# Kernel optimization log

Hardware: AMD Instinct MI355X
Metric: run time of the kernel (lower is better)

Reference implementation:

```python
import jax, jax.numpy as jnp
import numpy as np

ALPHA = 0.2          # leaky_relu negative slope
NEG_INF = -9e15      # mask fill value (matches torch source)


def setup_inputs() -> dict:
    key = jax.random.key(0)
    k_h, k_mask, k_W, k_a = jax.random.split(key, 4)
    B, N, F_in, F_out = 4, 65536, 128, 128
    h = jax.random.normal(k_h, (B, N, F_in), dtype=jnp.float32)
    # op_mask > 0 means "mask out this neighbor" (prev/self/next)
    op_mask = jax.random.randint(k_mask, (B, N, 3), 0, 2, dtype=jnp.int32)
    # xavier_uniform-style init for params
    lim_W = 1.414 * np.sqrt(6.0 / (F_in + F_out))
    W = jax.random.uniform(k_W, (F_in, F_out), dtype=jnp.float32, minval=-lim_W, maxval=lim_W)
    lim_a = 1.414 * np.sqrt(6.0 / (2 * F_out + 1))
    a = jax.random.uniform(k_a, (2 * F_out, 1), dtype=jnp.float32, minval=-lim_a, maxval=lim_a)
    return {"h": h, "op_mask": op_mask, "W": W, "a": a}


def reference(h, op_mask, W, a):
    F_out = W.shape[1]
    Wh = jnp.matmul(h, W)                                   # [B, N, F]
    # windowed neighbors: prev (roll +1), self, next (roll -1)
    Wh_concat = jnp.stack(
        [jnp.roll(Wh, 1, axis=1), Wh, jnp.roll(Wh, -1, axis=1)], axis=-2
    )                                                       # [B, N, 3, F]
    Wh1 = jnp.matmul(Wh, a[:F_out])                         # [B, N, 1]
    Wh2 = jnp.matmul(Wh, a[F_out:])                         # [B, N, 1]
    Wh2_concat = jnp.stack(
        [jnp.roll(Wh2, 1, axis=1), Wh2, jnp.roll(Wh2, -1, axis=1)], axis=-1
    )                                                       # [B, N, 1, 3]
    e = jax.nn.leaky_relu(Wh1[..., None] + Wh2_concat, ALPHA)  # [B, N, 1, 3]
    e = jnp.where(op_mask[:, :, None, :] > 0, jnp.float32(NEG_INF), e)
    attention = jax.nn.softmax(e, axis=-1)                  # [B, N, 1, 3]
    # dropout_prob = 0.0 (eval-equivalent), so dropout is identity
    h_new = jnp.matmul(attention, Wh_concat).squeeze(-2)    # [B, N, F]
    return h_new
```

## Files before the change

kernel.cpp:

```cpp
#include <hip/hip_runtime.h>
#include <hip/hip_bf16.h>

typedef __attribute__((ext_vector_type(8))) short short8;
typedef __attribute__((ext_vector_type(4))) float f32x4;

#define ALPHA 0.2f
#define NEG_INF -9e15f
#define OUT_ROWS 126

__device__ __forceinline__ unsigned short f2bf(float x) {
    union { float f; unsigned int u; } v; v.f = x;
    unsigned int r = v.u + 0x7FFFu + ((v.u >> 16) & 1u);
    return (unsigned short)(r >> 16);
}

__global__ __launch_bounds__(256, 2)
void gat_fused(const float* __restrict__ h, const int* __restrict__ opm,
               const float* __restrict__ W, const float* __restrict__ a,
               float* __restrict__ out, int N) {
    __shared__ __align__(16) char smem[65536];
    __shared__ float a_s[256];
    __shared__ float wh1_s[128];
    __shared__ float wh2_s[128];
    __shared__ float att_s[128][4];

    const int t = threadIdx.x;
    const int b = blockIdx.y;
    const int row_start = blockIdx.x * OUT_ROWS;
    const int out_rows = min(OUT_ROWS, N - row_start);
    const float* hB = h + (size_t)b * N * 128;
    float* outB = out + (size_t)b * N * 128;

    a_s[t] = a[t];

    #pragma unroll
    for (int i = 0; i < 16; ++i) {
        int idx4 = t + i * 256;
        int k = idx4 >> 5;
        int n4 = (idx4 & 31) << 2;
        float4 w4 = *(const float4*)(W + (k << 7) + n4);
        unsigned short bf[4] = { f2bf(w4.x), f2bf(w4.y), f2bf(w4.z), f2bf(w4.w) };
        #pragma unroll
        for (int j = 0; j < 4; ++j) {
            int jj = j ^ (t & 3);
            int n = n4 + jj;
            *(unsigned short*)(smem + 32768 + n * 256 + ((k * 2) ^ ((n & 7) << 4))) = bf[jj];
        }
    }
    #pragma unroll
    for (int i = 0; i < 16; ++i) {
        int idx4 = t + i * 256;
        int r = idx4 >> 5;
        int c = (idx4 & 31) << 2;
        int g = row_start - 1 + r;
        if (g < 0) g += N;
        if (g >= N) g -= N;
        float4 h4 = *(const float4*)(hB + (size_t)g * 128 + c);
        ushort4 p = make_ushort4(f2bf(h4.x), f2bf(h4.y), f2bf(h4.z), f2bf(h4.w));
        *(ushort4*)(smem + r * 256 + ((c * 2) ^ ((r & 7) << 4))) = p;
    }
    __syncthreads();

    const int lane = t & 63;
    const int wave = t >> 6;
    const int wr = (wave >> 1) << 6;
    const int wc = (wave & 1) << 6;
    const int l15 = lane & 15;
    const int lg = (lane >> 4) & 3;

    f32x4 acc[4][4];
    #pragma unroll
    for (int mi = 0; mi < 4; ++mi)
        #pragma unroll
        for (int ni = 0; ni < 4; ++ni)
            acc[mi][ni] = (f32x4){0.f, 0.f, 0.f, 0.f};

    #pragma unroll
    for (int kk = 0; kk < 4; ++kk) {
        int kbyte = (kk << 6) + (lg << 4);
        short8 af[4], bfr[4];
        #pragma unroll
        for (int mi = 0; mi < 4; ++mi) {
            int m = wr + (mi << 4) + l15;
            af[mi] = *(const short8*)(smem + m * 256 + (kbyte ^ ((m & 7) << 4)));
        }
        #pragma unroll
        for (int ni = 0; ni < 4; ++ni) {
            int n = wc + (ni << 4) + l15;
            bfr[ni] = *(const short8*)(smem + 32768 + n * 256 + (kbyte ^ ((n & 7) << 4)));
        }
        #pragma unroll
        for (int mi = 0; mi < 4; ++mi)
            #pragma unroll
            for (int ni = 0; ni < 4; ++ni)
                acc[mi][ni] = __builtin_amdgcn_mfma_f32_16x16x32_bf16(
                    af[mi], bfr[ni], acc[mi][ni], 0, 0, 0);
    }
    __syncthreads();

    #pragma unroll
    for (int mi = 0; mi < 4; ++mi) {
        #pragma unroll
        for (int ni = 0; ni < 4; ++ni) {
            int col = wc + (ni << 4) + l15;
            #pragma unroll
            for (int j = 0; j < 4; ++j) {
                int row = wr + (mi << 4) + (lg << 2) + j;
                *(float*)(smem + row * 512 + ((col * 4) ^ ((row & 7) << 4))) = acc[mi][ni][j];
            }
        }
    }
    __syncthreads();

    {
        int r = t >> 1;
        int cb = (t & 1) << 6;
        float s1 = 0.f, s2 = 0.f;
        #pragma unroll
        for (int i = 0; i < 16; ++i) {
            int c = cb + (i << 2);
            f32x4 w4 = *(const f32x4*)(smem + r * 512 + ((c * 4) ^ ((r & 7) << 4)));
            s1 += w4[0] * a_s[c] + w4[1] * a_s[c + 1] + w4[2] * a_s[c + 2] + w4[3] * a_s[c + 3];
            s2 += w4[0] * a_s[128 + c] + w4[1] * a_s[129 + c] + w4[2] * a_s[130 + c] + w4[3] * a_s[131 + c];
        }
        s1 += __shfl_xor(s1, 1);
        s2 += __shfl_xor(s2, 1);
        if ((t & 1) == 0) { wh1_s[r] = s1; wh2_s[r] = s2; }
    }
    __syncthreads();

    if (t < 128) {
        int r = t;
        if (r >= 1 && r <= out_rows) {
            int g = row_start + r - 1;
            const int* mr = opm + ((size_t)b * N + g) * 3;
            float w1 = wh1_s[r];
            float e0 = w1 + wh2_s[r - 1];
            float e1 = w1 + wh2_s[r];
            float e2 = w1 + wh2_s[r + 1];
            e0 = e0 > 0.f ? e0 : ALPHA * e0;
            e1 = e1 > 0.f ? e1 : ALPHA * e1;
            e2 = e2 > 0.f ? e2 : ALPHA * e2;
            if (mr[0] > 0) e0 = NEG_INF;
            if (mr[1] > 0) e1 = NEG_INF;
            if (mr[2] > 0) e2 = NEG_INF;
            float m = fmaxf(e0, fmaxf(e1, e2));
            float x0 = expf(e0 - m), x1 = expf(e1 - m), x2 = expf(e2 - m);
            float inv = 1.f / (x0 + x1 + x2);
            att_s[r][0] = x0 * inv;
            att_s[r][1] = x1 * inv;
            att_s[r][2] = x2 * inv;
        }
    }
    __syncthreads();

    for (int it = 0; it < 16; ++it) {
        int r = 1 + (wave << 1) + ((lane >> 5) & 1) + (it << 3);
        if (r > out_rows) continue;
        int c = (lane & 31) << 2;
        float a0 = att_s[r][0], a1 = att_s[r][1], a2 = att_s[r][2];
        f32x4 wm = *(const f32x4*)(smem + (r - 1) * 512 + ((c * 4) ^ (((r - 1) & 7) << 4)));
        f32x4 w0 = *(const f32x4*)(smem + r * 512 + ((c * 4) ^ ((r & 7) << 4)));
        f32x4 wp = *(const f32x4*)(smem + (r + 1) * 512 + ((c * 4) ^ (((r + 1) & 7) << 4)));
        f32x4 res;
        #pragma unroll
        for (int j = 0; j < 4; ++j)
            res[j] = a0 * wm[j] + a1 * w0[j] + a2 * wp[j];
        int g = row_start + r - 1;
        *(f32x4*)(outB + (size_t)g * 128 + c) = res;
    }
}

extern "C" void kernel_launch(void* const* d_in, const int* in_sizes, int n_in,
                              void* d_out, int out_size, void* d_ws, size_t ws_size,
                              hipStream_t stream) {
    const float* h   = (const float*)d_in[0];
    const int*   opm = (const int*)d_in[1];
    const float* W   = (const float*)d_in[2];
    const float* a   = (const float*)d_in[3];
    float* out = (float*)d_out;
    const int N = 65536;
    const int B = 4;
    dim3 grid((N + OUT_ROWS - 1) / OUT_ROWS, B);
    gat_fused<<<grid, 256, 0, stream>>>(h, opm, W, a, out, N);
}
```

Before: 65.04 us.

## Prepack W into MFMA fragment layout and store Wh as bf16 in LDS

A small pre-kernel converts W to bf16 once and writes it to the workspace in the exact per-lane MFMA B-fragment order. The main kernel then loads B fragments straight from global memory instead of having every block transpose W into shared memory. The Wh tile is stored back to LDS as bf16 rather than fp32, which halves LDS to 32KB and allows launch bounds of 4 blocks per CU instead of 2. In exchange it adds a second launch and per-block global reads of W fragments, and rounding Wh to bf16 before the attention reductions and output loses precision.

```diff
diff --git a/kernel.cpp b/kernel.cpp
--- a/kernel.cpp
+++ b/kernel.cpp
@@ -13,12 +13,31 @@
     unsigned int r = v.u + 0x7FFFu + ((v.u >> 16) & 1u);
     return (unsigned short)(r >> 16);
 }
+__device__ __forceinline__ float bf2f(unsigned short x) {
+    union { unsigned int u; float f; } v; v.u = ((unsigned int)x) << 16;
+    return v.f;
+}
 
-__global__ __launch_bounds__(256, 2)
+__global__ void prep_wt(const float* __restrict__ W, unsigned short* __restrict__ ws) {
+    int q = blockIdx.x * 256 + threadIdx.x;
+    int lane = q & 63;
+    int fi = q >> 6;
+    int ni = fi & 3;
+    int kk = (fi >> 2) & 3;
+    int wcg = fi >> 4;
+    int n = wcg * 64 + ni * 16 + (lane & 15);
+    int k0 = kk * 32 + ((lane >> 4) & 3) * 8;
+    short8 o;
+    #pragma unroll
+    for (int j = 0; j < 8; ++j) o[j] = (short)f2bf(W[(k0 + j) * 128 + n]);
+    *(short8*)(ws + (size_t)q * 8) = o;
+}
+
+__global__ __launch_bounds__(256, 4)
 void gat_fused(const float* __restrict__ h, const int* __restrict__ opm,
-               const float* __restrict__ W, const float* __restrict__ a,
+               const unsigned short* __restrict__ ws, const float* __restrict__ a,
                float* __restrict__ out, int N) {
-    __shared__ __align__(16) char smem[65536];
+    __shared__ __align__(16) char smem[32768];
     __shared__ float a_s[256];
     __shared__ float wh1_s[128];
     __shared__ float wh2_s[128];
@@ -36,20 +55,6 @@
     #pragma unroll
     for (int i = 0; i < 16; ++i) {
         int idx4 = t + i * 256;
-        int k = idx4 >> 5;
-        int n4 = (idx4 & 31) << 2;
-        float4 w4 = *(const float4*)(W + (k << 7) + n4);
-        unsigned short bf[4] = { f2bf(w4.x), f2bf(w4.y), f2bf(w4.z), f2bf(w4.w) };
-        #pragma unroll
-        for (int j = 0; j < 4; ++j) {
-            int jj = j ^ (t & 3);
-            int n = n4 + jj;
-            *(unsigned short*)(smem + 32768 + n * 256 + ((k * 2) ^ ((n & 7) << 4))) = bf[jj];
-        }
-    }
-    #pragma unroll
-    for (int i = 0; i < 16; ++i) {
-        int idx4 = t + i * 256;
         int r = idx4 >> 5;
         int c = (idx4 & 31) << 2;
         int g = row_start - 1 + r;
@@ -64,7 +69,8 @@
     const int lane = t & 63;
     const int wave = t >> 6;
     const int wr = (wave >> 1) << 6;
-    const int wc = (wave & 1) << 6;
+    const int wcg = wave & 1;
+    const int wc = wcg << 6;
     const int l15 = lane & 15;
     const int lg = (lane >> 4) & 3;
 
@@ -75,19 +81,18 @@
         for (int ni = 0; ni < 4; ++ni)
             acc[mi][ni] = (f32x4){0.f, 0.f, 0.f, 0.f};
 
+    const short8* wsv = (const short8*)ws;
     #pragma unroll
     for (int kk = 0; kk < 4; ++kk) {
         int kbyte = (kk << 6) + (lg << 4);
         short8 af[4], bfr[4];
         #pragma unroll
+        for (int ni = 0; ni < 4; ++ni)
+            bfr[ni] = wsv[(((wcg << 2) + kk) * 4 + ni) * 64 + lane];
+        #pragma unroll
         for (int mi = 0; mi < 4; ++mi) {
             int m = wr + (mi << 4) + l15;
             af[mi] = *(const short8*)(smem + m * 256 + (kbyte ^ ((m & 7) << 4)));
-        }
-        #pragma unroll
-        for (int ni = 0; ni < 4; ++ni) {
-            int n = wc + (ni << 4) + l15;
-            bfr[ni] = *(const short8*)(smem + 32768 + n * 256 + (kbyte ^ ((n & 7) << 4)));
         }
         #pragma unroll
         for (int mi = 0; mi < 4; ++mi)
@@ -106,7 +111,8 @@
             #pragma unroll
             for (int j = 0; j < 4; ++j) {
                 int row = wr + (mi << 4) + (lg << 2) + j;
-                *(float*)(smem + row * 512 + ((col * 4) ^ ((row & 7) << 4))) = acc[mi][ni][j];
+                *(unsigned short*)(smem + row * 256 + ((col * 2) ^ ((row & 7) << 4))) =
+                    f2bf(acc[mi][ni][j]);
             }
         }
     }
@@ -117,11 +123,15 @@
         int cb = (t & 1) << 6;
         float s1 = 0.f, s2 = 0.f;
         #pragma unroll
-        for (int i = 0; i < 16; ++i) {
-            int c = cb + (i << 2);
-            f32x4 w4 = *(const f32x4*)(smem + r * 512 + ((c * 4) ^ ((r & 7) << 4)));
-            s1 += w4[0] * a_s[c] + w4[1] * a_s[c + 1] + w4[2] * a_s[c + 2] + w4[3] * a_s[c + 3];
-            s2 += w4[0] * a_s[128 + c] + w4[1] * a_s[129 + c] + w4[2] * a_s[130 + c] + w4[3] * a_s[131 + c];
+        for (int i = 0; i < 8; ++i) {
+            int c = cb + (i << 3);
+            short8 wv = *(const short8*)(smem + r * 256 + ((c * 2) ^ ((r & 7) << 4)));
+            #pragma unroll
+            for (int j = 0; j < 8; ++j) {
+                float w = bf2f((unsigned short)wv[j]);
+                s1 += w * a_s[c + j];
+                s2 += w * a_s[128 + c + j];
+            }
         }
         s1 += __shfl_xor(s1, 1);
         s2 += __shfl_xor(s2, 1);
@@ -155,17 +165,18 @@
     __syncthreads();
 
     for (int it = 0; it < 16; ++it) {
-        int r = 1 + (wave << 1) + ((lane >> 5) & 1) + (it << 3);
+        int r = 1 + (t >> 5) + (it << 3);
         if (r > out_rows) continue;
-        int c = (lane & 31) << 2;
+        int c = (t & 31) << 2;
         float a0 = att_s[r][0], a1 = att_s[r][1], a2 = att_s[r][2];
-        f32x4 wm = *(const f32x4*)(smem + (r - 1) * 512 + ((c * 4) ^ (((r - 1) & 7) << 4)));
-        f32x4 w0 = *(const f32x4*)(smem + r * 512 + ((c * 4) ^ ((r & 7) << 4)));
-        f32x4 wp = *(const f32x4*)(smem + (r + 1) * 512 + ((c * 4) ^ (((r + 1) & 7) << 4)));
+        ushort4 wm = *(const ushort4*)(smem + (r - 1) * 256 + ((c * 2) ^ (((r - 1) & 7) << 4)));
+        ushort4 w0 = *(const ushort4*)(smem + r * 256 + ((c * 2) ^ ((r & 7) << 4)));
+        ushort4 wp = *(const ushort4*)(smem + (r + 1) * 256 + ((c * 2) ^ (((r + 1) & 7) << 4)));
         f32x4 res;
-        #pragma unroll
-        for (int j = 0; j < 4; ++j)
-            res[j] = a0 * wm[j] + a1 * w0[j] + a2 * wp[j];
+        res[0] = a0 * bf2f(wm.x) + a1 * bf2f(w0.x) + a2 * bf2f(wp.x);
+        res[1] = a0 * bf2f(wm.y) + a1 * bf2f(w0.y) + a2 * bf2f(wp.y);
+        res[2] = a0 * bf2f(wm.z) + a1 * bf2f(w0.z) + a2 * bf2f(wp.z);
+        res[3] = a0 * bf2f(wm.w) + a1 * bf2f(w0.w) + a2 * bf2f(wp.w);
         int g = row_start + r - 1;
         *(f32x4*)(outB + (size_t)g * 128 + c) = res;
     }
@@ -179,8 +190,10 @@
     const float* W   = (const float*)d_in[2];
     const float* a   = (const float*)d_in[3];
     float* out = (float*)d_out;
+    unsigned short* ws = (unsigned short*)d_ws;
     const int N = 65536;
     const int B = 4;
+    prep_wt<<<8, 256, 0, stream>>>(W, ws);
     dim3 grid((N + OUT_ROWS - 1) / OUT_ROWS, B);
-    gat_fused<<<grid, 256, 0, stream>>>(h, opm, W, a, out, N);
+    gat_fused<<<grid, 256, 0, stream>>>(h, opm, ws, a, out, N);
 }
```

After: 65.28 us. No clear change (+0.4%).
